# Optimization experiments

Hardware: AMD Instinct MI355X
Metric: run time of the kernel (lower is better)

The kernel has to match this reference:

```python
import jax, jax.numpy as jnp
import numpy as np
import math

N, LQ, C = 4, 5440, 256
H, L, P = 8, 4, 4
D = C // H
SHAPES = [(64, 64), (32, 32), (16, 16), (8, 8)]
STARTS = [0, 4096, 5120, 5376]
LEN_IN = 5440


def setup_inputs() -> dict:
    key = jax.random.key(0)
    ks = jax.random.split(key, 12)
    s = 1.0 / math.sqrt(C)
    return {
        "query": jax.random.normal(ks[0], (N, LQ, C), jnp.float32),
        "reference_points": jax.random.uniform(ks[1], (N, LQ, L, 2), jnp.float32),
        "input_flatten": jax.random.normal(ks[2], (N, LEN_IN, C), jnp.float32),
        "input_spatial_shapes": jnp.asarray(SHAPES, jnp.int32),
        "input_level_start_index": jnp.asarray(STARTS, jnp.int32),
        "w_off": jax.random.normal(ks[3], (C, H * L * P * 2), jnp.float32) * 0.01,
        "b_off": jax.random.normal(ks[4], (H * L * P * 2,), jnp.float32) * 0.5,
        "w_attn": jax.random.normal(ks[5], (C, H * L * P), jnp.float32) * 0.01,
        "b_attn": jnp.zeros((H * L * P,), jnp.float32),
        "w_val": jax.random.normal(ks[6], (C, C), jnp.float32) * s,
        "b_val": jnp.zeros((C,), jnp.float32),
        "w_out": jax.random.normal(ks[7], (C, C), jnp.float32) * s,
        "b_out": jnp.zeros((C,), jnp.float32),
    }


def _gather_corner(lv, yi, xi, w):
    # lv: (N, h*w, H, D); yi, xi: (N, Lq, H, P) int32 -> (N, Lq, H, P, D)
    n, lq, h_, p_ = yi.shape
    idx = yi * w + xi
    idx2 = idx.transpose(0, 1, 3, 2).reshape(n, lq * p_, h_)[..., None]
    g = jnp.take_along_axis(lv, idx2, axis=1)  # (N, Lq*P, H, D)
    return g.reshape(n, lq, p_, h_, -1).transpose(0, 1, 3, 2, 4)


def _msdeform(query, reference_points, input_flatten, shapes, starts,
              w_off, b_off, w_attn, b_attn, w_val, b_val, w_out, b_out):
    n, lq, c = query.shape
    value = (input_flatten @ w_val + b_val).reshape(n, -1, H, D)
    off = (query @ w_off + b_off).reshape(n, lq, H, L, P, 2)
    attn = jax.nn.softmax((query @ w_attn + b_attn).reshape(n, lq, H, L * P), axis=-1)
    # sampling locations in [0,1], (N, Lq, H, L, P, 2)
    loc = jnp.clip(reference_points[:, :, None, :, None, :] + off, 0.0, 1.0)
    sampled = []
    for lvl, (hh, ww) in enumerate(shapes):
        s0 = starts[lvl]
        lv = value[:, s0:s0 + hh * ww]  # (N, hh*ww, H, D)
        xy = loc[:, :, :, lvl] * jnp.asarray([ww, hh], jnp.float32) - 0.5  # (N,Lq,H,P,2)
        x, y = xy[..., 0], xy[..., 1]
        x0 = jnp.floor(x)
        y0 = jnp.floor(y)
        x0i = jnp.clip(x0.astype(jnp.int32), 0, ww - 1)
        x1i = jnp.clip(x0.astype(jnp.int32) + 1, 0, ww - 1)
        y0i = jnp.clip(y0.astype(jnp.int32), 0, hh - 1)
        y1i = jnp.clip(y0.astype(jnp.int32) + 1, 0, hh - 1)
        x0f, x1f = x0i.astype(x.dtype), x1i.astype(x.dtype)
        y0f, y1f = y0i.astype(y.dtype), y1i.astype(y.dtype)
        wa = ((x1f - x) * (y1f - y))[..., None]
        wb = ((x1f - x) * (y - y0f))[..., None]
        wc = ((x - x0f) * (y1f - y))[..., None]
        wd = ((x - x0f) * (y - y0f))[..., None]
        va = _gather_corner(lv, y0i, x0i, ww)
        vb = _gather_corner(lv, y1i, x0i, ww)
        vc = _gather_corner(lv, y0i, x1i, ww)
        vd = _gather_corner(lv, y1i, x1i, ww)
        sampled.append(wa * va + wb * vb + wc * vc + wd * vd)
    sampled = jnp.concatenate(sampled, axis=3)  # (N, Lq, H, L*P, D)
    out = jnp.einsum('nqhp,nqhpd->nqhd', attn, sampled).reshape(n, lq, c)
    return out @ w_out + b_out


def reference(query, reference_points, input_flatten, input_spatial_shapes,
              input_level_start_index, w_off, b_off, w_attn, b_attn,
              w_val, b_val, w_out, b_out):
    shapes = [tuple(int(v) for v in row) for row in np.asarray(input_spatial_shapes)]
    starts = [int(v) for v in np.asarray(input_level_start_index)]
    return _msdeform(query, reference_points, input_flatten, shapes, starts,
                     w_off, b_off, w_attn, b_attn, w_val, b_val, w_out, b_out)
```

## Files before the change

### kernel.cpp

```cpp
#include <hip/hip_runtime.h>
#include <hip/hip_fp16.h>
#include <math.h>

#define C_DIM 256
#define H_DIM 8
#define L_DIM 4
#define P_DIM 4
#define LQ 5440
#define LEN_IN 5440
#define NB 4
#define M_ROWS (NB * LQ)
#define NPANEL64 (M_ROWS / 64)

typedef __attribute__((ext_vector_type(8))) _Float16 f16x8;
typedef __attribute__((ext_vector_type(8))) unsigned short u16x8;
typedef __attribute__((ext_vector_type(4))) float f32x4;

__device__ __forceinline__ void split_f32(float a, __half& h, __half& l) {
    h = __float2half(a);
    l = __float2half(a - __half2float(h));
}

__global__ __launch_bounds__(256) void convert_all(const float* __restrict__ w_val,
                                                   const float* __restrict__ w_off,
                                                   const float* __restrict__ w_attn,
                                                   const float* __restrict__ w_out,
                                                   const float* __restrict__ b_off,
                                                   const float* __restrict__ b_attn,
                                                   __half* __restrict__ wv_hi, __half* __restrict__ wv_lo,
                                                   __half* __restrict__ wc_hi, __half* __restrict__ wc_lo,
                                                   __half* __restrict__ wt_hi, __half* __restrict__ wt_lo,
                                                   float* __restrict__ bc) {
    const int b = blockIdx.x, k = threadIdx.x;
    if (b < 896) {
        const float* w; __half *hi, *lo; int ncols, col, orow;
        if (b < 256)      { w = w_val;  hi = wv_hi; lo = wv_lo; ncols = 256; col = b;       orow = col; }
        else if (b < 512) { w = w_off;  hi = wc_hi; lo = wc_lo; ncols = 256; col = b - 256; orow = col; }
        else if (b < 640) { w = w_attn; hi = wc_hi; lo = wc_lo; ncols = 128; col = b - 512; orow = col + 256; }
        else              { w = w_out;  hi = wt_hi; lo = wt_lo; ncols = 256; col = b - 640; orow = col; }
        const float a = w[(size_t)k * ncols + col];
        __half h, l;
        split_f32(a, h, l);
        hi[(size_t)orow * 256 + k] = h;
        lo[(size_t)orow * 256 + k] = l;
    } else if (b == 896) {
        bc[k] = b_off[k];
    } else {
        if (k < 128) bc[256 + k] = b_attn[k];
    }
}

template <int NC>
__global__ __launch_bounds__(256, 4) void gemm_f16x3(const float* __restrict__ A,
                                                     const __half* __restrict__ Bhi,
                                                     const __half* __restrict__ Blo,
                                                     const float* __restrict__ bias,
                                                     float* __restrict__ outp) {
    constexpr int NX = NC / 64;

    __shared__ __align__(16) __half sA[2][64][32];
    __shared__ __align__(16) __half sB[2][64][32];
    __shared__ __align__(16) float sepi[4][16][32];

    const int bid = blockIdx.x;
    const int c = bid & 7;
    const int rest = bid >> 3;
    const int x = rest % NX;
    const int yg = rest / NX;
    const int y = yg * 8 + c;
    if (y >= NPANEL64) return;

    const int n0 = x * 64;
    const int row0 = y * 64;
    const int t = threadIdx.x;
    const int w = t >> 6, lane = t & 63;
    const int bm = (w >> 1) * 32, bn = (w & 1) * 32;
    const int fr = lane & 15;
    const int fc = lane >> 4;

    const int ar = t >> 2;
    const int ak8 = t & 3;
    const int asw = (ak8 ^ ((ar >> 1) & 3)) * 8;
    const int br = t >> 2;
    const int bc8 = t & 3;
    const int bsw = (bc8 ^ ((br >> 1) & 3)) * 8;

    const size_t ga = (size_t)(row0 + ar) * 256 + ak8 * 8;
    const size_t gb = (size_t)(n0 + br) * 256 + bc8 * 8;

    f32x4 acc[2][2];
#pragma unroll
    for (int m = 0; m < 2; ++m)
#pragma unroll
        for (int n = 0; n < 2; ++n)
#pragma unroll
            for (int r = 0; r < 4; ++r) acc[m][n][r] = 0.f;

    float4 pa[2], pb[2];
    pa[0] = *(const float4*)(A + ga);
    pa[1] = *(const float4*)(A + ga + 4);
    pb[0] = *(const float4*)(Bhi + gb);
    pb[1] = *(const float4*)(Blo + gb);

    for (int kt = 0; kt < 8; ++kt) {
        if (kt) __syncthreads();
        {
            const float4 u = pa[0], v = pa[1];
            const float e[8] = {u.x, u.y, u.z, u.w, v.x, v.y, v.z, v.w};
            u16x8 Hh, Ll;
#pragma unroll
            for (int i = 0; i < 8; ++i) {
                __half h, l;
                split_f32(e[i], h, l);
                Hh[i] = __half_as_ushort(h);
                Ll[i] = __half_as_ushort(l);
            }
            *(u16x8*)&sA[0][ar][asw] = Hh;
            *(u16x8*)&sA[1][ar][asw] = Ll;
        }
        *(float4*)&sB[0][br][bsw] = pb[0];
        *(float4*)&sB[1][br][bsw] = pb[1];
        __syncthreads();
        if (kt < 7) {
            const size_t ko = (size_t)(kt + 1) * 32;
            pa[0] = *(const float4*)(A + ga + ko);
            pa[1] = *(const float4*)(A + ga + ko + 4);
            pb[0] = *(const float4*)(Bhi + gb + ko);
            pb[1] = *(const float4*)(Blo + gb + ko);
        }

        f16x8 bhf[2], blf[2];
#pragma unroll
        for (int n = 0; n < 2; ++n) {
            const int rowb = bn + n * 16 + fr;
            const int swb = (fc ^ ((rowb >> 1) & 3)) * 8;
            bhf[n] = *(const f16x8*)&sB[0][rowb][swb];
            blf[n] = *(const f16x8*)&sB[1][rowb][swb];
        }
#pragma unroll
        for (int m = 0; m < 2; ++m) {
            const int rowa = bm + m * 16 + fr;
            const int swa = (fc ^ ((rowa >> 1) & 3)) * 8;
            const f16x8 ah = *(const f16x8*)&sA[0][rowa][swa];
            const f16x8 al = *(const f16x8*)&sA[1][rowa][swa];
#pragma unroll
            for (int n = 0; n < 2; ++n) {
                acc[m][n] = __builtin_amdgcn_mfma_f32_16x16x32_f16(ah, bhf[n], acc[m][n], 0, 0, 0);
                acc[m][n] = __builtin_amdgcn_mfma_f32_16x16x32_f16(al, bhf[n], acc[m][n], 0, 0, 0);
                acc[m][n] = __builtin_amdgcn_mfma_f32_16x16x32_f16(ah, blf[n], acc[m][n], 0, 0, 0);
            }
        }
    }

    float bv[2];
#pragma unroll
    for (int n = 0; n < 2; ++n) bv[n] = bias[n0 + bn + n * 16 + fr];

#pragma unroll
    for (int m = 0; m < 2; ++m) {
#pragma unroll
        for (int n = 0; n < 2; ++n) {
            const int kch = n * 4 + (fr >> 2);
            const int lo4 = fr & 3;
#pragma unroll
            for (int r = 0; r < 4; ++r) {
                const int rw = fc * 4 + r;
                const int sk = (kch ^ (rw & 7)) & 7;
                sepi[w][rw][sk * 4 + lo4] = acc[m][n][r] + bv[n];
            }
        }
#pragma unroll
        for (int jj = 0; jj < 2; ++jj) {
            const int flat = jj * 64 + lane;
            const int rw = flat >> 3;
            const int k = flat & 7;
            const int sk = (k ^ (rw & 7)) & 7;
            const float4 vv = *(const float4*)&sepi[w][rw][sk * 4];
            const int grow = row0 + bm + m * 16 + rw;
            *(float4*)&outp[(size_t)grow * NC + (n0 + bn + k * 4)] = vv;
        }
    }
}

__global__ __launch_bounds__(256) void sample_kernel(const float* __restrict__ value,
                                                     const float* __restrict__ ol,
                                                     const float* __restrict__ refpts,
                                                     float* __restrict__ tmp) {
    const int t = threadIdx.x;
    const int w = t >> 6, lane = t & 63;

    __shared__ __align__(16) float4 s_aw[4][128];
    __shared__ __align__(16) uint4 s_of[4][128];

    const int h = lane >> 3;
    const unsigned l16 = (unsigned)(lane * 16);

    const int bid = blockIdx.x;
    const int xcd = bid & 7;
    const int pos = bid >> 3;
    const int n = xcd >> 1;
    const int qgrp = (xcd & 1) * 340 + pos;

    const char* vbn = (const char*)value + (size_t)n * (LEN_IN * C_DIM * 4);

    for (int it = 0; it < 2; ++it) {
        const int q = n * LQ + qgrp * 8 + w * 2 + it;

#pragma unroll
        for (int s = 0; s < 2; ++s) {
            const int j = lane + 64 * s;
            const int hq = j >> 4, lp = j & 15;
            const int l = lp >> 2;
            const int ww = 64 >> l;
            int st = 0;
            if (l == 1) st = 4096;
            else if (l == 2) st = 5120;
            else if (l == 3) st = 5376;

            const float2 oxy = *(const float2*)&ol[(size_t)q * 384 + 2 * j];
            const float2 rxy = *(const float2*)&refpts[((size_t)q * L_DIM + l) * 2];

            const float fw = (float)ww;
            const float x = fminf(fmaxf(rxy.x + oxy.x, 0.f), 1.f) * fw - 0.5f;
            const float y = fminf(fmaxf(rxy.y + oxy.y, 0.f), 1.f) * fw - 0.5f;
            const int xi = (int)floorf(x);
            const int yi = (int)floorf(y);
            const int x0i = min(max(xi, 0), ww - 1);
            const int x1i = min(max(xi + 1, 0), ww - 1);
            const int y0i = min(max(yi, 0), ww - 1);
            const int y1i = min(max(yi + 1, 0), ww - 1);
            const float wx0 = (float)x1i - x, wx1 = x - (float)x0i;
            const float wy0 = (float)y1i - y, wy1 = y - (float)y0i;

            const float lg = ol[(size_t)q * 384 + 256 + j];
            float m = lg;
#pragma unroll
            for (int o = 8; o; o >>= 1) m = fmaxf(m, __shfl_xor(m, o, 16));
            const float e = expf(lg - m);
            float sm = e;
#pragma unroll
            for (int o = 8; o; o >>= 1) sm += __shfl_xor(sm, o, 16);
            const float a = e / sm;

            const int p = lp * 8 + (hq ^ (lp & 7));
            float4 aw;
            aw.x = a * (wx0 * wy0);
            aw.y = a * (wx0 * wy1);
            aw.z = a * (wx1 * wy0);
            aw.w = a * (wx1 * wy1);
            uint4 of;
            of.x = (unsigned)(st + y0i * ww + x0i) << 10;
            of.y = (unsigned)(st + y1i * ww + x0i) << 10;
            of.z = (unsigned)(st + y0i * ww + x1i) << 10;
            of.w = (unsigned)(st + y1i * ww + x1i) << 10;
            s_aw[w][p] = aw;
            s_of[w][p] = of;
        }

        float4 acc;
        acc.x = 0.f; acc.y = 0.f; acc.z = 0.f; acc.w = 0.f;
#pragma unroll
        for (int lp = 0; lp < 16; ++lp) {
            const int p = lp * 8 + (h ^ (lp & 7));
            const float4 aw = s_aw[w][p];
            const uint4 of = s_of[w][p];
            const float4 v0 = *(const float4*)(vbn + (of.x + l16));
            const float4 v1 = *(const float4*)(vbn + (of.y + l16));
            const float4 v2 = *(const float4*)(vbn + (of.z + l16));
            const float4 v3 = *(const float4*)(vbn + (of.w + l16));
            acc.x += aw.x * v0.x + aw.y * v1.x + aw.z * v2.x + aw.w * v3.x;
            acc.y += aw.x * v0.y + aw.y * v1.y + aw.z * v2.y + aw.w * v3.y;
            acc.z += aw.x * v0.z + aw.y * v1.z + aw.z * v2.z + aw.w * v3.z;
            acc.w += aw.x * v0.w + aw.y * v1.w + aw.z * v2.w + aw.w * v3.w;
        }
        *(float4*)&tmp[(size_t)q * 256 + (size_t)(lane * 4)] = acc;
    }
}

extern "C" void kernel_launch(void* const* d_in, const int* in_sizes, int n_in,
                              void* d_out, int out_size, void* d_ws, size_t ws_size,
                              hipStream_t stream) {
    const float* query         = (const float*)d_in[0];
    const float* refpts        = (const float*)d_in[1];
    const float* input_flatten = (const float*)d_in[2];
    const float* w_off  = (const float*)d_in[5];
    const float* b_off  = (const float*)d_in[6];
    const float* w_attn = (const float*)d_in[7];
    const float* b_attn = (const float*)d_in[8];
    const float* w_val  = (const float*)d_in[9];
    const float* b_val  = (const float*)d_in[10];
    const float* w_out  = (const float*)d_in[11];
    const float* b_out  = (const float*)d_in[12];
    float* out = (float*)d_out;

    const size_t nr = (size_t)M_ROWS;
    float* p = (float*)d_ws;
    float* value_ws = p; p += nr * 256;
    float* ol_ws    = p; p += nr * 384;
    float* tmp_ws   = p; p += nr * 256;
    float* bc_ws    = p; p += 384;
    __half* wv_hi = (__half*)p;
    __half* wv_lo = wv_hi + 256 * 256;
    __half* wc_hi = wv_lo + 256 * 256;
    __half* wc_lo = wc_hi + 384 * 256;
    __half* wt_hi = wc_lo + 384 * 256;
    __half* wt_lo = wt_hi + 256 * 256;

    convert_all<<<898, 256, 0, stream>>>(w_val, w_off, w_attn, w_out, b_off, b_attn,
                                         wv_hi, wv_lo, wc_hi, wc_lo, wt_hi, wt_lo, bc_ws);

    const int g256 = 8 * 4 * 43;
    const int g384 = 8 * 6 * 43;

    gemm_f16x3<256><<<g256, 256, 0, stream>>>(input_flatten, wv_hi, wv_lo, b_val, value_ws);
    gemm_f16x3<384><<<g384, 256, 0, stream>>>(query, wc_hi, wc_lo, bc_ws, ol_ws);

    sample_kernel<<<M_ROWS / 8, 256, 0, stream>>>(value_ws, ol_ws, refpts, tmp_ws);

    gemm_f16x3<256><<<g256, 256, 0, stream>>>(tmp_ws, wt_hi, wt_lo, b_out, out);
}
```

Measured before the change: 172.7 us.

## Enlarge GEMM tiles to 128x64 with K-step 64 and reuse LDS for epilogue

```diff
diff --git a/kernel.cpp b/kernel.cpp
--- a/kernel.cpp
+++ b/kernel.cpp
@@ -10,7 +10,7 @@
 #define LEN_IN 5440
 #define NB 4
 #define M_ROWS (NB * LQ)
-#define NPANEL64 (M_ROWS / 64)
+#define NPANEL (M_ROWS / 128)
 
 typedef __attribute__((ext_vector_type(8))) _Float16 f16x8;
 typedef __attribute__((ext_vector_type(8))) unsigned short u16x8;
@@ -51,113 +51,124 @@
 }
 
 template <int NC>
-__global__ __launch_bounds__(256, 4) void gemm_f16x3(const float* __restrict__ A,
+__global__ __launch_bounds__(256, 3) void gemm_f16x3(const float* __restrict__ A,
                                                      const __half* __restrict__ Bhi,
                                                      const __half* __restrict__ Blo,
                                                      const float* __restrict__ bias,
                                                      float* __restrict__ outp) {
-    constexpr int NX = NC / 64;
-
-    __shared__ __align__(16) __half sA[2][64][32];
-    __shared__ __align__(16) __half sB[2][64][32];
-    __shared__ __align__(16) float sepi[4][16][32];
-
-    const int bid = blockIdx.x;
-    const int c = bid & 7;
-    const int rest = bid >> 3;
-    const int x = rest % NX;
-    const int yg = rest / NX;
-    const int y = yg * 8 + c;
-    if (y >= NPANEL64) return;
-
-    const int n0 = x * 64;
-    const int row0 = y * 64;
+    __shared__ __align__(16) __half sA[2][128][64];
+    __shared__ __align__(16) __half sB[2][64][64];
+
+    const int n0 = blockIdx.x * 64;
+    const int row0 = blockIdx.y * 128;
     const int t = threadIdx.x;
     const int w = t >> 6, lane = t & 63;
-    const int bm = (w >> 1) * 32, bn = (w & 1) * 32;
+    const int bm = (w >> 1) * 64, bn = (w & 1) * 32;
     const int fr = lane & 15;
     const int fc = lane >> 4;
 
-    const int ar = t >> 2;
-    const int ak8 = t & 3;
-    const int asw = (ak8 ^ ((ar >> 1) & 3)) * 8;
+    const int ar = t >> 1;
+    const int ag0 = (t & 1) * 4;
     const int br = t >> 2;
-    const int bc8 = t & 3;
-    const int bsw = (bc8 ^ ((br >> 1) & 3)) * 8;
-
-    const size_t ga = (size_t)(row0 + ar) * 256 + ak8 * 8;
-    const size_t gb = (size_t)(n0 + br) * 256 + bc8 * 8;
-
-    f32x4 acc[2][2];
-#pragma unroll
-    for (int m = 0; m < 2; ++m)
+    const int bg0 = (t & 3) * 2;
+
+    const float* Ap = A + (size_t)(row0 + ar) * 256 + ag0 * 8;
+    const __half* Bh = Bhi + (size_t)(n0 + br) * 256 + bg0 * 8;
+    const __half* Bl = Blo + (size_t)(n0 + br) * 256 + bg0 * 8;
+
+    f32x4 acc[4][2];
+#pragma unroll
+    for (int m = 0; m < 4; ++m)
 #pragma unroll
         for (int n = 0; n < 2; ++n)
 #pragma unroll
             for (int r = 0; r < 4; ++r) acc[m][n][r] = 0.f;
 
-    float4 pa[2], pb[2];
-    pa[0] = *(const float4*)(A + ga);
-    pa[1] = *(const float4*)(A + ga + 4);
-    pb[0] = *(const float4*)(Bhi + gb);
-    pb[1] = *(const float4*)(Blo + gb);
-
-    for (int kt = 0; kt < 8; ++kt) {
+    float4 pa[8];
+    float4 pb[4];
+#pragma unroll
+    for (int i = 0; i < 4; ++i) {
+        pa[2 * i]     = *(const float4*)(Ap + i * 8);
+        pa[2 * i + 1] = *(const float4*)(Ap + i * 8 + 4);
+    }
+    pb[0] = *(const float4*)(Bh);
+    pb[1] = *(const float4*)(Bh + 8);
+    pb[2] = *(const float4*)(Bl);
+    pb[3] = *(const float4*)(Bl + 8);
+
+    for (int kt = 0; kt < 4; ++kt) {
         if (kt) __syncthreads();
-        {
-            const float4 u = pa[0], v = pa[1];
+#pragma unroll
+        for (int i = 0; i < 4; ++i) {
+            const float4 u = pa[2 * i], v = pa[2 * i + 1];
             const float e[8] = {u.x, u.y, u.z, u.w, v.x, v.y, v.z, v.w};
             u16x8 Hh, Ll;
 #pragma unroll
-            for (int i = 0; i < 8; ++i) {
+            for (int j = 0; j < 8; ++j) {
                 __half h, l;
-                split_f32(e[i], h, l);
-                Hh[i] = __half_as_ushort(h);
-                Ll[i] = __half_as_ushort(l);
-            }
-            *(u16x8*)&sA[0][ar][asw] = Hh;
-            *(u16x8*)&sA[1][ar][asw] = Ll;
-        }
-        *(float4*)&sB[0][br][bsw] = pb[0];
-        *(float4*)&sB[1][br][bsw] = pb[1];
+                split_f32(e[j], h, l);
+                Hh[j] = __half_as_ushort(h);
+                Ll[j] = __half_as_ushort(l);
+            }
+            const int sw = ((ag0 + i) ^ (ar & 7)) * 8;
+            *(u16x8*)&sA[0][ar][sw] = Hh;
+            *(u16x8*)&sA[1][ar][sw] = Ll;
+        }
+#pragma unroll
+        for (int i = 0; i < 2; ++i) {
+            const int sw = ((bg0 + i) ^ (br & 7)) * 8;
+            *(float4*)&sB[0][br][sw] = pb[i];
+            *(float4*)&sB[1][br][sw] = pb[2 + i];
+        }
         __syncthreads();
-        if (kt < 7) {
-            const size_t ko = (size_t)(kt + 1) * 32;
-            pa[0] = *(const float4*)(A + ga + ko);
-            pa[1] = *(const float4*)(A + ga + ko + 4);
-            pb[0] = *(const float4*)(Bhi + gb + ko);
-            pb[1] = *(const float4*)(Blo + gb + ko);
-        }
-
-        f16x8 bhf[2], blf[2];
-#pragma unroll
-        for (int n = 0; n < 2; ++n) {
-            const int rowb = bn + n * 16 + fr;
-            const int swb = (fc ^ ((rowb >> 1) & 3)) * 8;
-            bhf[n] = *(const f16x8*)&sB[0][rowb][swb];
-            blf[n] = *(const f16x8*)&sB[1][rowb][swb];
-        }
-#pragma unroll
-        for (int m = 0; m < 2; ++m) {
-            const int rowa = bm + m * 16 + fr;
-            const int swa = (fc ^ ((rowa >> 1) & 3)) * 8;
-            const f16x8 ah = *(const f16x8*)&sA[0][rowa][swa];
-            const f16x8 al = *(const f16x8*)&sA[1][rowa][swa];
+        if (kt < 3) {
+            const size_t ko = (size_t)(kt + 1) * 64;
+#pragma unroll
+            for (int i = 0; i < 4; ++i) {
+                pa[2 * i]     = *(const float4*)(Ap + ko + i * 8);
+                pa[2 * i + 1] = *(const float4*)(Ap + ko + i * 8 + 4);
+            }
+            pb[0] = *(const float4*)(Bh + ko);
+            pb[1] = *(const float4*)(Bh + ko + 8);
+            pb[2] = *(const float4*)(Bl + ko);
+            pb[3] = *(const float4*)(Bl + ko + 8);
+        }
+
+#pragma unroll
+        for (int kk = 0; kk < 2; ++kk) {
+            f16x8 bhf[2], blf[2];
 #pragma unroll
             for (int n = 0; n < 2; ++n) {
-                acc[m][n] = __builtin_amdgcn_mfma_f32_16x16x32_f16(ah, bhf[n], acc[m][n], 0, 0, 0);
-                acc[m][n] = __builtin_amdgcn_mfma_f32_16x16x32_f16(al, bhf[n], acc[m][n], 0, 0, 0);
-                acc[m][n] = __builtin_amdgcn_mfma_f32_16x16x32_f16(ah, blf[n], acc[m][n], 0, 0, 0);
-            }
-        }
-    }
+                const int rowb = bn + n * 16 + fr;
+                const int cb = ((kk * 4 + fc) ^ (rowb & 7)) * 8;
+                bhf[n] = *(const f16x8*)&sB[0][rowb][cb];
+                blf[n] = *(const f16x8*)&sB[1][rowb][cb];
+            }
+#pragma unroll
+            for (int m = 0; m < 4; ++m) {
+                const int rowa = bm + m * 16 + fr;
+                const int ca = ((kk * 4 + fc) ^ (rowa & 7)) * 8;
+                const f16x8 ah = *(const f16x8*)&sA[0][rowa][ca];
+                const f16x8 al = *(const f16x8*)&sA[1][rowa][ca];
+#pragma unroll
+                for (int n = 0; n < 2; ++n) {
+                    acc[m][n] = __builtin_amdgcn_mfma_f32_16x16x32_f16(ah, bhf[n], acc[m][n], 0, 0, 0);
+                    acc[m][n] = __builtin_amdgcn_mfma_f32_16x16x32_f16(al, bhf[n], acc[m][n], 0, 0, 0);
+                    acc[m][n] = __builtin_amdgcn_mfma_f32_16x16x32_f16(ah, blf[n], acc[m][n], 0, 0, 0);
+                }
+            }
+        }
+    }
+
+    __syncthreads();
+    float (*sepi)[16][32] = reinterpret_cast<float (*)[16][32]>(&sA[0][0][0]);
 
     float bv[2];
 #pragma unroll
     for (int n = 0; n < 2; ++n) bv[n] = bias[n0 + bn + n * 16 + fr];
 
 #pragma unroll
-    for (int m = 0; m < 2; ++m) {
+    for (int m = 0; m < 4; ++m) {
 #pragma unroll
         for (int n = 0; n < 2; ++n) {
             const int kch = n * 4 + (fr >> 2);
@@ -309,8 +320,8 @@
     convert_all<<<898, 256, 0, stream>>>(w_val, w_off, w_attn, w_out, b_off, b_attn,
                                          wv_hi, wv_lo, wc_hi, wc_lo, wt_hi, wt_lo, bc_ws);
 
-    const int g256 = 8 * 4 * 43;
-    const int g384 = 8 * 6 * 43;
+    dim3 g256(4, M_ROWS / 128);
+    dim3 g384(6, M_ROWS / 128);
 
     gemm_f16x3<256><<<g256, 256, 0, stream>>>(input_flatten, wv_hi, wv_lo, b_val, value_ws);
     gemm_f16x3<384><<<g384, 256, 0, stream>>>(query, wc_hi, wc_lo, bc_ws, ol_ws);
```

After: 172.3 us. No clear change (-0.3%).
